# Performance work log

Hardware: AMD Instinct MI355X
Metric: run time of the kernel (lower is better)

Reference implementation:

```python
import jax, jax.numpy as jnp
import numpy as np

B, M, N = 32, 512, 512
XD = YD = 512   # x_size, y_size
S = 512         # shared_size
H = 512         # hidden_size
MAXD = 11       # max relative distance


def _lin(k, i, o):
    lim = float(np.sqrt(6.0 / (i + o)))  # xavier_uniform, gain=1
    return jax.random.uniform(k, (i, o), jnp.float32, -lim, lim)


def setup_inputs() -> dict:
    key = jax.random.key(0)
    ks = jax.random.split(key, 16)
    inp = {
        'prem': jax.random.normal(ks[0], (B, M, YD), jnp.float32),
        'hypo': jax.random.normal(ks[1], (B, N, XD), jnp.float32),
        'prem_mask': jnp.ones((B, M), dtype=bool),
        'hypo_mask': jnp.ones((B, N), dtype=bool),
        # projections
        'Wpx': _lin(ks[2], XD, S), 'bpx': jnp.zeros((S,), jnp.float32),
        'Wpy': _lin(ks[3], YD, S), 'bpy': jnp.zeros((S,), jnp.float32),
        # relative-distance bias embedding (2*max_dist+1, squeezed to scalar)
        'dist_embed': jax.random.normal(ks[4], (2 * MAXD + 1,), jnp.float32),
        # self-attention DeepDot MLP: S -> H -> H
        'Ws1': _lin(ks[5], S, H), 'bs1': jnp.zeros((H,), jnp.float32),
        'Ws2': _lin(ks[6], H, H), 'bs2': jnp.zeros((H,), jnp.float32),
        # cross-attention DeepDot MLP: 2S -> H -> H
        'Wa1': _lin(ks[7], 2 * S, H), 'ba1': jnp.zeros((H,), jnp.float32),
        'Wa2': _lin(ks[8], H, H), 'ba2': jnp.zeros((H,), jnp.float32),
        # compare layer: 4S -> H -> H
        'Wc1': _lin(ks[9], 4 * S, H), 'bc1': jnp.zeros((H,), jnp.float32),
        'Wc2': _lin(ks[10], H, H), 'bc2': jnp.zeros((H,), jnp.float32),
        # aggregate layer: 2H -> H -> H
        'Wg1': _lin(ks[11], 2 * H, H), 'bg1': jnp.zeros((H,), jnp.float32),
        'Wg2': _lin(ks[12], H, H), 'bg2': jnp.zeros((H,), jnp.float32),
    }
    return inp


def _mlp2(x, W1, b1, W2, b2):
    # Linear -> ReLU -> Linear -> ReLU (dropout=0.0)
    h = jax.nn.relu(x @ W1 + b1)
    return jax.nn.relu(h @ W2 + b2)


def _rel_bias(size, dist_embed):
    v = jnp.arange(size)
    d = jnp.clip(v[None, :] - v[:, None], -MAXD, MAXD) + MAXD  # [size,size]
    return dist_embed[d]


def _masked_softmax(t, mask):
    # mask True = valid; broadcast over query dim
    return jax.nn.softmax(jnp.where(mask, t, -jnp.inf), axis=-1)


def reference(prem, hypo, prem_mask, hypo_mask,
              Wpx, bpx, Wpy, bpy, dist_embed,
              Ws1, bs1, Ws2, bs2,
              Wa1, ba1, Wa2, ba2,
              Wc1, bc1, Wc2, bc2,
              Wg1, bg1, Wg2, bg2):
    hypo_p = hypo @ Wpx + bpx   # [B,N,S]
    prem_p = prem @ Wpy + bpy   # [B,M,S]

    # self attention (DeepDot: shared MLP on q and k, then qk^T)
    fp = _mlp2(prem_p, Ws1, bs1, Ws2, bs2)
    fh = _mlp2(hypo_p, Ws1, bs1, Ws2, bs2)
    p_scores = jnp.einsum('bmh,bnh->bmn', fp, fp) + _rel_bias(prem_p.shape[1], dist_embed)[None]
    h_scores = jnp.einsum('bmh,bnh->bmn', fh, fh) + _rel_bias(hypo_p.shape[1], dist_embed)[None]

    p_att = _masked_softmax(p_scores, prem_mask[:, None, :])
    h_att = _masked_softmax(h_scores, hypo_mask[:, None, :])
    prem_ctx = jnp.einsum('bmn,bnd->bmd', p_att, prem_p)
    hypo_ctx = jnp.einsum('bmn,bnd->bmd', h_att, hypo_p)

    prem2 = jnp.concatenate([prem_p, prem_ctx], axis=-1)  # [B,M,2S]
    hypo2 = jnp.concatenate([hypo_p, hypo_ctx], axis=-1)  # [B,N,2S]

    # cross attention
    gp = _mlp2(prem2, Wa1, ba1, Wa2, ba2)
    gh = _mlp2(hypo2, Wa1, ba1, Wa2, ba2)
    sim = jnp.einsum('bmh,bnh->bmn', gp, gh)  # [B,M,N]
    p2h = _masked_softmax(sim, hypo_mask[:, None, :])
    h2p = _masked_softmax(jnp.swapaxes(sim, 1, 2), prem_mask[:, None, :])
    attended_hypo = jnp.einsum('bmn,bnd->bmd', p2h, hypo2)  # [B,M,2S]
    attended_prem = jnp.einsum('bnm,bmd->bnd', h2p, prem2)  # [B,N,2S]

    prem_cmp = _mlp2(jnp.concatenate([prem2, attended_hypo], -1), Wc1, bc1, Wc2, bc2)
    hypo_cmp = _mlp2(jnp.concatenate([hypo2, attended_prem], -1), Wc1, bc1, Wc2, bc2)

    prem_cmp = (prem_cmp * prem_mask[..., None].astype(prem_cmp.dtype)).sum(axis=1)  # [B,H]
    hypo_cmp = (hypo_cmp * hypo_mask[..., None].astype(hypo_cmp.dtype)).sum(axis=1)  # [B,H]

    return _mlp2(jnp.concatenate([prem_cmp, hypo_cmp], -1), Wg1, bg1, Wg2, bg2)
```

## Files before the change

kernel.cpp:

```cpp
#include <hip/hip_runtime.h>
#include <hip/hip_bf16.h>


typedef __bf16 bf16x8 __attribute__((ext_vector_type(8)));
typedef float floatx16 __attribute__((ext_vector_type(16)));

__device__ __forceinline__ unsigned short f32_to_bf16(float f) {
    unsigned int u = __float_as_uint(f);
    unsigned int r = (u + 0x7FFFu + ((u >> 16) & 1u)) >> 16;
    return (unsigned short)r;
}
__device__ __forceinline__ float bf16_to_f32(unsigned short h) {
    return __uint_as_float(((unsigned int)h) << 16);
}

__global__ __launch_bounds__(256) void cvt_kernel(const float* __restrict__ X,
                                                  unsigned short* __restrict__ Y,
                                                  long long n4) {
    long long i = ((long long)blockIdx.x * blockDim.x + threadIdx.x);
    if (i < n4) {
        float4 f = ((const float4*)X)[i];
        ushort4 o;
        o.x = f32_to_bf16(f.x); o.y = f32_to_bf16(f.y);
        o.z = f32_to_bf16(f.z); o.w = f32_to_bf16(f.w);
        ((ushort4*)Y)[i] = o;
    }
}

__global__ __launch_bounds__(256) void transpose_w_kernel(const float* __restrict__ W,
                                                          unsigned short* __restrict__ Wt,
                                                          int K, int N) {
    __shared__ unsigned short tile[32][33];
    int n0 = blockIdx.x * 32, k0 = blockIdx.y * 32;
    int tx = threadIdx.x & 31, ty = threadIdx.x >> 5;
    #pragma unroll
    for (int i = 0; i < 4; ++i) {
        int ky = ty + i * 8;
        tile[ky][tx] = f32_to_bf16(W[(long long)(k0 + ky) * N + n0 + tx]);
    }
    __syncthreads();
    #pragma unroll
    for (int i = 0; i < 4; ++i) {
        int ny = ty + i * 8;
        Wt[(long long)(n0 + ny) * K + k0 + tx] = tile[tx][ny];
    }
}

template <bool BT>
__global__ __launch_bounds__(256, 4) void gemm_kernel(
    const unsigned short* __restrict__ A, int lda, long long strideA,
    const unsigned short* __restrict__ B, int ldb, long long strideB,
    float* __restrict__ C32, unsigned short* __restrict__ Cb, int ldc, long long strideC,
    const float* __restrict__ bias, int relu, int M, int N, int K,
    float* __restrict__ csum, int swz) {
    constexpr int BBYTES = BT ? 8192 : (32 * 264);
    constexpr int BUF = 8192 + BBYTES;
    __shared__ alignas(16) char smem[2 * BUF];

    const int t = threadIdx.x;
    const int lane = t & 63;
    const int wave = t >> 6;
    const int wm = (wave >> 1) * 64;
    const int wn = (wave & 1) * 64;
    const int ln = lane & 31;
    const int h = lane >> 5;

    int bx = blockIdx.x, by = blockIdx.y;
    if (swz) {
        int Nt = gridDim.x, Mt = gridDim.y;
        int L = by * Nt + bx;
        int x = L & 7, s = L >> 3;
        by = x * (Mt >> 3) + s / Nt;
        bx = s % Nt;
    }
    const int m0 = by * 128;
    const int n0 = bx * 128;
    const int bz = blockIdx.z;

    const unsigned short* aptr = A + (long long)bz * strideA +
                                 (long long)(m0 + (t >> 1)) * lda + (t & 1) * 16;
    const unsigned short* bptr;
    if (BT)
        bptr = B + (long long)bz * strideB +
               (long long)(n0 + (t >> 1)) * ldb + (t & 1) * 16;
    else
        bptr = B + (long long)bz * strideB +
               (long long)(t >> 4) * ldb + n0 + (t & 15) * 8;
    const long long bstep = BT ? 8 : 16 * (long long)ldb;

    const int aoff = ((t & 1) * 256 + (t >> 1)) * 16;
    const int boff = BT ? (8192 + ((t & 1) * 256 + (t >> 1)) * 16)
                        : (8192 + (t >> 4) * 264 + (t & 15) * 16);
    const int boff2 = BT ? 2048 : 16 * 264;

    floatx16 acc[2][2];
    #pragma unroll
    for (int im = 0; im < 2; ++im)
        #pragma unroll
        for (int in = 0; in < 2; ++in)
            acc[im][in] = (floatx16)(0.f);

    uint4 va0 = *(const uint4*)(aptr);
    uint4 va1 = *(const uint4*)(aptr + 8);
    uint4 vb0 = *(const uint4*)(bptr);
    uint4 vb1 = *(const uint4*)(bptr + bstep);
    aptr += 32;
    bptr += BT ? 32 : 32 * (long long)ldb;
    *(uint4*)(smem + aoff) = va0;
    *(uint4*)(smem + aoff + 2048) = va1;
    *(uint4*)(smem + boff) = vb0;
    *(uint4*)(smem + boff + boff2) = vb1;
    va0 = *(const uint4*)(aptr);
    va1 = *(const uint4*)(aptr + 8);
    vb0 = *(const uint4*)(bptr);
    vb1 = *(const uint4*)(bptr + bstep);
    aptr += 32;
    bptr += BT ? 32 : 32 * (long long)ldb;
    __syncthreads();

    int p = 0;
    for (int k0 = 0; k0 < K; k0 += 32) {
        const char* base = smem + p * BUF;
        #pragma unroll
        for (int s = 0; s < 2; ++s) {
            bf16x8 a[2], b[2];
            #pragma unroll
            for (int im = 0; im < 2; ++im)
                a[im] = *(const bf16x8*)(base + ((s * 2 + h) * 128 + wm + im * 32 + ln) * 16);
            if (BT) {
                #pragma unroll
                for (int in = 0; in < 2; ++in)
                    b[in] = *(const bf16x8*)(base + 8192 +
                                             ((s * 2 + h) * 128 + wn + in * 32 + ln) * 16);
            } else {
                #pragma unroll
                for (int in = 0; in < 2; ++in) {
                    union { bf16x8 v; unsigned short u[8]; } u;
                    #pragma unroll
                    for (int j = 0; j < 8; ++j)
                        u.u[j] = *(const unsigned short*)(base + 8192 +
                                 (s * 16 + h * 8 + j) * 264 + (wn + in * 32 + ln) * 2);
                    b[in] = u.v;
                }
            }
            #pragma unroll
            for (int im = 0; im < 2; ++im)
                #pragma unroll
                for (int in = 0; in < 2; ++in)
                    acc[im][in] = __builtin_amdgcn_mfma_f32_32x32x16_bf16(
                        a[im], b[in], acc[im][in], 0, 0, 0);
        }

        if (k0 + 32 < K) {
            char* nb = smem + (p ^ 1) * BUF;
            *(uint4*)(nb + aoff) = va0;
            *(uint4*)(nb + aoff + 2048) = va1;
            *(uint4*)(nb + boff) = vb0;
            *(uint4*)(nb + boff + boff2) = vb1;
            if (k0 + 64 < K) {
                va0 = *(const uint4*)(aptr);
                va1 = *(const uint4*)(aptr + 8);
                vb0 = *(const uint4*)(bptr);
                vb1 = *(const uint4*)(bptr + bstep);
                aptr += 32;
                bptr += BT ? 32 : 32 * (long long)ldb;
            }
            __syncthreads();
            p ^= 1;
        }
    }

    if (csum) {
        const int bidx = m0 >> 9;
        const long long cbase = (long long)(bidx & 31) * 1024 + (bidx >> 5) * 512;
        #pragma unroll
        for (int in = 0; in < 2; ++in) {
            int n = n0 + wn + in * 32 + ln;
            float bn = bias ? bias[n] : 0.f;
            float s = 0.f;
            #pragma unroll
            for (int im = 0; im < 2; ++im)
                #pragma unroll
                for (int r = 0; r < 16; ++r) {
                    float v = acc[im][in][r] + bn;
                    if (relu) v = fmaxf(v, 0.f);
                    s += v;
                }
            s += __shfl_xor(s, 32);
            if (lane < 32) atomicAdd(&csum[cbase + n], s);
        }
        return;
    }

    float* C32b = C32 ? C32 + (long long)bz * strideC : nullptr;
    unsigned short* Cbb = Cb ? Cb + (long long)bz * strideC : nullptr;
    #pragma unroll
    for (int im = 0; im < 2; ++im) {
        #pragma unroll
        for (int in = 0; in < 2; ++in) {
            int n = n0 + wn + in * 32 + ln;
            float bn = bias ? bias[n] : 0.f;
            #pragma unroll
            for (int r = 0; r < 16; ++r) {
                int m = m0 + wm + im * 32 + (r & 3) + 8 * (r >> 2) + 4 * h;
                float v = acc[im][in][r] + bn;
                if (relu) v = fmaxf(v, 0.f);
                long long off = (long long)m * ldc + n;
                if (C32b) C32b[off] = v;
                if (Cbb) Cbb[off] = f32_to_bf16(v);
            }
        }
    }
}

__global__ __launch_bounds__(256) void softmax_kernel(const float* __restrict__ S,
                                                      unsigned short* __restrict__ P,
                                                      const float* __restrict__ de,
                                                      int rel, int N) {
    const int row = blockIdx.x;
    const int b = blockIdx.y;
    const long long base = ((long long)b * gridDim.x + row) * N;
    const int t = threadIdx.x;
    const int lane = t & 63, wv = t >> 6;
    __shared__ float redmax[4], redsum[4];

    float v[2];
    float mx = -1e30f;
    #pragma unroll
    for (int i = 0; i < 2; ++i) {
        int c = t + i * 256;
        float x = S[base + c];
        if (rel) {
            int d = c - row;
            d = min(11, max(-11, d));
            x += de[d + 11];
        }
        v[i] = x;
        mx = fmaxf(mx, x);
    }
    #pragma unroll
    for (int o = 32; o > 0; o >>= 1) mx = fmaxf(mx, __shfl_down(mx, o));
    if (lane == 0) redmax[wv] = mx;
    __syncthreads();
    mx = fmaxf(fmaxf(redmax[0], redmax[1]), fmaxf(redmax[2], redmax[3]));

    float s = 0.f;
    #pragma unroll
    for (int i = 0; i < 2; ++i) { v[i] = __expf(v[i] - mx); s += v[i]; }
    #pragma unroll
    for (int o = 32; o > 0; o >>= 1) s += __shfl_down(s, o);
    if (lane == 0) redsum[wv] = s;
    __syncthreads();
    s = redsum[0] + redsum[1] + redsum[2] + redsum[3];
    float inv = 1.f / s;
    #pragma unroll
    for (int i = 0; i < 2; ++i) P[base + t + i * 256] = f32_to_bf16(v[i] * inv);
}

__global__ __launch_bounds__(512) void mlp_agg_kernel(const float* __restrict__ X,
                                                      const float* __restrict__ W,
                                                      const float* __restrict__ bias,
                                                      float* __restrict__ out,
                                                      int K, int N, int relu) {
    const int b = blockIdx.y;
    const int nl = threadIdx.x & 63;
    const int n = blockIdx.x * 64 + nl;
    const int ks = threadIdx.x >> 6;
    const int kchunk = K >> 3;
    const float* Xb = X + (long long)b * K;
    const int k0 = ks * kchunk;
    float s = 0.f;
    #pragma unroll 8
    for (int k = k0; k < k0 + kchunk; ++k)
        s += Xb[k] * W[(long long)k * N + n];
    __shared__ float red[8][64];
    red[ks][nl] = s;
    __syncthreads();
    if (threadIdx.x < 64) {
        float t = 0.f;
        #pragma unroll
        for (int i = 0; i < 8; ++i) t += red[i][threadIdx.x];
        t += bias[n];
        if (relu) t = fmaxf(t, 0.f);
        out[(long long)b * N + n] = t;
    }
}

static void gemm(hipStream_t st, bool bt,
                 const void* A, int lda, long long sA,
                 const void* B, int ldb, long long sB,
                 float* C32, void* Cb, int ldc, long long sC,
                 const float* bias, int relu, int M, int N, int K, int batch,
                 float* csum = nullptr) {
    dim3 g(N / 128, M / 128, batch), blk(256);
    int swz = (batch == 1 && (M / 128) % 8 == 0) ? 1 : 0;
    if (bt)
        gemm_kernel<true><<<g, blk, 0, st>>>((const unsigned short*)A, lda, sA,
                                             (const unsigned short*)B, ldb, sB,
                                             C32, (unsigned short*)Cb, ldc, sC, bias, relu, M, N, K,
                                             csum, swz);
    else
        gemm_kernel<false><<<g, blk, 0, st>>>((const unsigned short*)A, lda, sA,
                                              (const unsigned short*)B, ldb, sB,
                                              C32, (unsigned short*)Cb, ldc, sC, bias, relu, M, N, K,
                                              csum, swz);
}

extern "C" void kernel_launch(void* const* d_in, const int* in_sizes, int n_in,
                              void* d_out, int out_size, void* d_ws, size_t ws_size,
                              hipStream_t stream) {
    const int B = 32, SEQ = 512, S = 512;
    const int MT = B * SEQ;
    const int M2 = 2 * MT;

    const float* prem = (const float*)d_in[0];
    const float* hypo = (const float*)d_in[1];
    const float* Wpx = (const float*)d_in[4];  const float* bpx = (const float*)d_in[5];
    const float* Wpy = (const float*)d_in[6];  const float* bpy = (const float*)d_in[7];
    const float* de  = (const float*)d_in[8];
    const float* Ws1 = (const float*)d_in[9];  const float* bs1 = (const float*)d_in[10];
    const float* Ws2 = (const float*)d_in[11]; const float* bs2 = (const float*)d_in[12];
    const float* Wa1 = (const float*)d_in[13]; const float* ba1 = (const float*)d_in[14];
    const float* Wa2 = (const float*)d_in[15]; const float* ba2 = (const float*)d_in[16];
    const float* Wc1 = (const float*)d_in[17]; const float* bc1 = (const float*)d_in[18];
    const float* Wc2 = (const float*)d_in[19]; const float* bc2 = (const float*)d_in[20];
    const float* Wg1 = (const float*)d_in[21]; const float* bg1 = (const float*)d_in[22];
    const float* Wg2 = (const float*)d_in[23]; const float* bg2 = (const float*)d_in[24];

    char* p = (char*)d_ws;
    auto alloc = [&](size_t bytes) { char* r = p; p += (bytes + 255) & ~(size_t)255; return r; };
    unsigned short* prem_bf = (unsigned short*)alloc((size_t)MT * S * 2);
    unsigned short* hypo_bf = (unsigned short*)alloc((size_t)MT * S * 2);
    unsigned short* premcat = (unsigned short*)alloc((size_t)MT * 2048 * 2);
    unsigned short* hypocat = (unsigned short*)alloc((size_t)MT * 2048 * 2);
    float* scores = (float*)alloc((size_t)B * SEQ * SEQ * 4);
    unsigned short* h1 = (unsigned short*)scores;
    unsigned short* att = (unsigned short*)alloc((size_t)B * SEQ * SEQ * 2);
    unsigned short* Wpx_t = (unsigned short*)alloc(512 * 512 * 2);
    unsigned short* Wpy_t = (unsigned short*)alloc(512 * 512 * 2);
    unsigned short* Ws1_t = (unsigned short*)alloc(512 * 512 * 2);
    unsigned short* Ws2_t = (unsigned short*)alloc(512 * 512 * 2);
    unsigned short* Wa1_t = (unsigned short*)alloc(512 * 1024 * 2);
    unsigned short* Wa2_t = (unsigned short*)alloc(512 * 512 * 2);
    unsigned short* Wc1_t = (unsigned short*)alloc(512 * 2048 * 2);
    unsigned short* Wc2_t = (unsigned short*)alloc(512 * 512 * 2);
    float* agg  = (float*)alloc(32 * 1024 * 4);
    float* aggh = (float*)alloc(32 * 512 * 4);

    const long long sBM = (long long)SEQ * SEQ;
    const long long sCat = (long long)SEQ * 2048;

    {
        long long n4 = (long long)MT * S / 4;
        cvt_kernel<<<dim3((n4 + 255) / 256), dim3(256), 0, stream>>>(prem, prem_bf, n4);
        cvt_kernel<<<dim3((n4 + 255) / 256), dim3(256), 0, stream>>>(hypo, hypo_bf, n4);
        transpose_w_kernel<<<dim3(16, 16), 256, 0, stream>>>(Wpx, Wpx_t, 512, 512);
        transpose_w_kernel<<<dim3(16, 16), 256, 0, stream>>>(Wpy, Wpy_t, 512, 512);
        transpose_w_kernel<<<dim3(16, 16), 256, 0, stream>>>(Ws1, Ws1_t, 512, 512);
        transpose_w_kernel<<<dim3(16, 16), 256, 0, stream>>>(Ws2, Ws2_t, 512, 512);
        transpose_w_kernel<<<dim3(16, 32), 256, 0, stream>>>(Wa1, Wa1_t, 1024, 512);
        transpose_w_kernel<<<dim3(16, 16), 256, 0, stream>>>(Wa2, Wa2_t, 512, 512);
        transpose_w_kernel<<<dim3(16, 64), 256, 0, stream>>>(Wc1, Wc1_t, 2048, 512);
        transpose_w_kernel<<<dim3(16, 16), 256, 0, stream>>>(Wc2, Wc2_t, 512, 512);
        hipMemsetAsync(agg, 0, 32 * 1024 * sizeof(float), stream);
    }

    gemm(stream, true, prem_bf, 512, 0, Wpy_t, 512, 0, nullptr, premcat, 2048, 0, bpy, 0, MT, 512, 512, 1);
    gemm(stream, true, hypo_bf, 512, 0, Wpx_t, 512, 0, nullptr, hypocat, 2048, 0, bpx, 0, MT, 512, 512, 1);

    gemm(stream, true, premcat, 2048, 0, Ws1_t, 512, 0, nullptr, h1, 512, 0, bs1, 1, M2, 512, 512, 1);
    gemm(stream, true, h1, 512, 0, Ws2_t, 512, 0, nullptr, prem_bf, 512, 0, bs2, 1, M2, 512, 512, 1);

    gemm(stream, true, prem_bf, 512, sBM, prem_bf, 512, sBM, scores, nullptr, 512, sBM, nullptr, 0, 512, 512, 512, B);
    softmax_kernel<<<dim3(512, B), 256, 0, stream>>>(scores, att, de, 1, 512);
    gemm(stream, false, att, 512, sBM, premcat, 2048, sCat, nullptr, premcat + 512, 2048, sCat,
         nullptr, 0, 512, 512, 512, B);

    gemm(stream, true, hypo_bf, 512, sBM, hypo_bf, 512, sBM, scores, nullptr, 512, sBM, nullptr, 0, 512, 512, 512, B);
    softmax_kernel<<<dim3(512, B), 256, 0, stream>>>(scores, att, de, 1, 512);
    gemm(stream, false, att, 512, sBM, hypocat, 2048, sCat, nullptr, hypocat + 512, 2048, sCat,
         nullptr, 0, 512, 512, 512, B);

    gemm(stream, true, premcat, 2048, 0, Wa1_t, 1024, 0, nullptr, h1, 512, 0, ba1, 1, M2, 512, 1024, 1);
    gemm(stream, true, h1, 512, 0, Wa2_t, 512, 0, nullptr, prem_bf, 512, 0, ba2, 1, M2, 512, 512, 1);

    gemm(stream, true, prem_bf, 512, sBM, hypo_bf, 512, sBM, scores, nullptr, 512, sBM, nullptr, 0, 512, 512, 512, B);
    softmax_kernel<<<dim3(512, B), 256, 0, stream>>>(scores, att, de, 0, 512);
    gemm(stream, false, att, 512, sBM, hypocat, 2048, sCat, nullptr, premcat + 1024, 2048, sCat,
         nullptr, 0, 512, 1024, 512, B);

    gemm(stream, true, hypo_bf, 512, sBM, prem_bf, 512, sBM, scores, nullptr, 512, sBM, nullptr, 0, 512, 512, 512, B);
    softmax_kernel<<<dim3(512, B), 256, 0, stream>>>(scores, att, de, 0, 512);
    gemm(stream, false, att, 512, sBM, premcat, 2048, sCat, nullptr, hypocat + 1024, 2048, sCat,
         nullptr, 0, 512, 1024, 512, B);

    gemm(stream, true, premcat, 2048, 0, Wc1_t, 2048, 0, nullptr, h1, 512, 0, bc1, 1, M2, 512, 2048, 1);
    gemm(stream, true, h1, 512, 0, Wc2_t, 512, 0, nullptr, nullptr, 512, 0, bc2, 1, M2, 512, 512, 1,
         agg);

    mlp_agg_kernel<<<dim3(8, 32), 512, 0, stream>>>(agg, Wg1, bg1, aggh, 1024, 512, 1);
    mlp_agg_kernel<<<dim3(8, 32), 512, 0, stream>>>(aggh, Wg2, bg2, (float*)d_out, 512, 512, 1);
}
```

Baseline: 773.2 us.

## Merge prem/hypo attention paths into batched launches and fuse fp32 input conversion

Removes the separate fp32-to-bf16 conversion kernels by letting the projection GEMM read fp32 activations directly and convert while staging to shared memory, with an M-split selecting the per-half weight and bias. Premise and hypothesis self- and cross-attention now run as single 64-batch GEMM and softmax launches, using a batch XOR offset to pair each premise with its hypothesis. The eight weight transposes are folded into one launch. The attention buffer now aliases the scores buffer, with each bf16 row written in place at double stride. This cuts launch count and tail effects, but relies on the in-place aliasing being safe and adds fp32 load bandwidth inside the GEMM.

```diff
diff --git a/kernel.cpp b/kernel.cpp
--- a/kernel.cpp
+++ b/kernel.cpp
@@ -10,33 +10,26 @@
     unsigned int r = (u + 0x7FFFu + ((u >> 16) & 1u)) >> 16;
     return (unsigned short)r;
 }
-__device__ __forceinline__ float bf16_to_f32(unsigned short h) {
-    return __uint_as_float(((unsigned int)h) << 16);
-}
-
-__global__ __launch_bounds__(256) void cvt_kernel(const float* __restrict__ X,
-                                                  unsigned short* __restrict__ Y,
-                                                  long long n4) {
-    long long i = ((long long)blockIdx.x * blockDim.x + threadIdx.x);
-    if (i < n4) {
-        float4 f = ((const float4*)X)[i];
-        ushort4 o;
-        o.x = f32_to_bf16(f.x); o.y = f32_to_bf16(f.y);
-        o.z = f32_to_bf16(f.z); o.w = f32_to_bf16(f.w);
-        ((ushort4*)Y)[i] = o;
-    }
-}
-
-__global__ __launch_bounds__(256) void transpose_w_kernel(const float* __restrict__ W,
-                                                          unsigned short* __restrict__ Wt,
-                                                          int K, int N) {
+
+struct TW {
+    const float* src[8];
+    unsigned short* dst[8];
+    int K[8];
+};
+__global__ __launch_bounds__(256) void transpose_all_kernel(TW tw) {
+    const int z = blockIdx.z;
+    const int K = tw.K[z];
+    const int k0 = blockIdx.y * 32;
+    if (k0 >= K) return;
+    const float* W = tw.src[z];
+    unsigned short* Wt = tw.dst[z];
     __shared__ unsigned short tile[32][33];
-    int n0 = blockIdx.x * 32, k0 = blockIdx.y * 32;
+    int n0 = blockIdx.x * 32;
     int tx = threadIdx.x & 31, ty = threadIdx.x >> 5;
     #pragma unroll
     for (int i = 0; i < 4; ++i) {
         int ky = ty + i * 8;
-        tile[ky][tx] = f32_to_bf16(W[(long long)(k0 + ky) * N + n0 + tx]);
+        tile[ky][tx] = f32_to_bf16(W[(long long)(k0 + ky) * 512 + n0 + tx]);
     }
     __syncthreads();
     #pragma unroll
@@ -46,10 +39,11 @@
     }
 }
 
-template <bool BT>
+template <bool BT, bool AF32>
 __global__ __launch_bounds__(256, 4) void gemm_kernel(
-    const unsigned short* __restrict__ A, int lda, long long strideA,
-    const unsigned short* __restrict__ B, int ldb, long long strideB,
+    const void* __restrict__ Av, const void* __restrict__ A2v, int lda, long long strideA,
+    const unsigned short* __restrict__ Bw, int ldb, long long strideB, int bxor,
+    const unsigned short* __restrict__ B2, const float* __restrict__ bias2, int Msplit,
     float* __restrict__ C32, unsigned short* __restrict__ Cb, int ldc, long long strideC,
     const float* __restrict__ bias, int relu, int M, int N, int K,
     float* __restrict__ csum, int swz) {
@@ -76,15 +70,31 @@
     const int m0 = by * 128;
     const int n0 = bx * 128;
     const int bz = blockIdx.z;
-
-    const unsigned short* aptr = A + (long long)bz * strideA +
-                                 (long long)(m0 + (t >> 1)) * lda + (t & 1) * 16;
+    const int bzB = (bz + bxor) & ((int)gridDim.z - 1);
+
+    const unsigned short* B = Bw;
+    const float* biasp = bias;
+    long long mA = m0;
+    if (Msplit && m0 >= Msplit) {
+        if (B2) B = B2;
+        if (bias2) biasp = bias2;
+        if (A2v) { Av = A2v; mA = m0 - Msplit; }
+    }
+
+    const float* aptrF = nullptr;
+    const unsigned short* aptrH = nullptr;
+    if constexpr (AF32)
+        aptrF = (const float*)Av + (long long)bz * strideA +
+                (mA + (t >> 1)) * (long long)lda + (t & 1) * 16;
+    else
+        aptrH = (const unsigned short*)Av + (long long)bz * strideA +
+                (mA + (t >> 1)) * (long long)lda + (t & 1) * 16;
     const unsigned short* bptr;
     if (BT)
-        bptr = B + (long long)bz * strideB +
+        bptr = B + (long long)bzB * strideB +
                (long long)(n0 + (t >> 1)) * ldb + (t & 1) * 16;
     else
-        bptr = B + (long long)bz * strideB +
+        bptr = B + (long long)bzB * strideB +
                (long long)(t >> 4) * ldb + n0 + (t & 15) * 8;
     const long long bstep = BT ? 8 : 16 * (long long)ldb;
 
@@ -100,22 +110,51 @@
         for (int in = 0; in < 2; ++in)
             acc[im][in] = (floatx16)(0.f);
 
-    uint4 va0 = *(const uint4*)(aptr);
-    uint4 va1 = *(const uint4*)(aptr + 8);
-    uint4 vb0 = *(const uint4*)(bptr);
-    uint4 vb1 = *(const uint4*)(bptr + bstep);
-    aptr += 32;
-    bptr += BT ? 32 : 32 * (long long)ldb;
-    *(uint4*)(smem + aoff) = va0;
-    *(uint4*)(smem + aoff + 2048) = va1;
-    *(uint4*)(smem + boff) = vb0;
-    *(uint4*)(smem + boff + boff2) = vb1;
-    va0 = *(const uint4*)(aptr);
-    va1 = *(const uint4*)(aptr + 8);
-    vb0 = *(const uint4*)(bptr);
-    vb1 = *(const uint4*)(bptr + bstep);
-    aptr += 32;
-    bptr += BT ? 32 : 32 * (long long)ldb;
+    uint4 va0, va1, vb0, vb1;
+    float4 fa0, fa1, fa2, fa3;
+
+    auto loadA = [&]() {
+        if constexpr (AF32) {
+            fa0 = *(const float4*)(aptrF);
+            fa1 = *(const float4*)(aptrF + 4);
+            fa2 = *(const float4*)(aptrF + 8);
+            fa3 = *(const float4*)(aptrF + 12);
+            aptrF += 32;
+        } else {
+            va0 = *(const uint4*)(aptrH);
+            va1 = *(const uint4*)(aptrH + 8);
+            aptrH += 32;
+        }
+    };
+    auto loadB = [&]() {
+        vb0 = *(const uint4*)(bptr);
+        vb1 = *(const uint4*)(bptr + bstep);
+        bptr += BT ? 32 : 32 * (long long)ldb;
+    };
+    auto commit = [&](char* buf) {
+        if constexpr (AF32) {
+            union { uint4 q; unsigned short u[8]; } c0, c1;
+            c0.u[0] = f32_to_bf16(fa0.x); c0.u[1] = f32_to_bf16(fa0.y);
+            c0.u[2] = f32_to_bf16(fa0.z); c0.u[3] = f32_to_bf16(fa0.w);
+            c0.u[4] = f32_to_bf16(fa1.x); c0.u[5] = f32_to_bf16(fa1.y);
+            c0.u[6] = f32_to_bf16(fa1.z); c0.u[7] = f32_to_bf16(fa1.w);
+            c1.u[0] = f32_to_bf16(fa2.x); c1.u[1] = f32_to_bf16(fa2.y);
+            c1.u[2] = f32_to_bf16(fa2.z); c1.u[3] = f32_to_bf16(fa2.w);
+            c1.u[4] = f32_to_bf16(fa3.x); c1.u[5] = f32_to_bf16(fa3.y);
+            c1.u[6] = f32_to_bf16(fa3.z); c1.u[7] = f32_to_bf16(fa3.w);
+            *(uint4*)(buf + aoff) = c0.q;
+            *(uint4*)(buf + aoff + 2048) = c1.q;
+        } else {
+            *(uint4*)(buf + aoff) = va0;
+            *(uint4*)(buf + aoff + 2048) = va1;
+        }
+        *(uint4*)(buf + boff) = vb0;
+        *(uint4*)(buf + boff + boff2) = vb1;
+    };
+
+    loadA(); loadB();
+    commit(smem);
+    loadA(); loadB();
     __syncthreads();
 
     int p = 0;
@@ -152,19 +191,8 @@
         }
 
         if (k0 + 32 < K) {
-            char* nb = smem + (p ^ 1) * BUF;
-            *(uint4*)(nb + aoff) = va0;
-            *(uint4*)(nb + aoff + 2048) = va1;
-            *(uint4*)(nb + boff) = vb0;
-            *(uint4*)(nb + boff + boff2) = vb1;
-            if (k0 + 64 < K) {
-                va0 = *(const uint4*)(aptr);
-                va1 = *(const uint4*)(aptr + 8);
-                vb0 = *(const uint4*)(bptr);
-                vb1 = *(const uint4*)(bptr + bstep);
-                aptr += 32;
-                bptr += BT ? 32 : 32 * (long long)ldb;
-            }
+            commit(smem + (p ^ 1) * BUF);
+            if (k0 + 64 < K) { loadA(); loadB(); }
             __syncthreads();
             p ^= 1;
         }
@@ -176,7 +204,7 @@
         #pragma unroll
         for (int in = 0; in < 2; ++in) {
             int n = n0 + wn + in * 32 + ln;
-            float bn = bias ? bias[n] : 0.f;
+            float bn = biasp ? biasp[n] : 0.f;
             float s = 0.f;
             #pragma unroll
             for (int im = 0; im < 2; ++im)
@@ -199,7 +227,7 @@
         #pragma unroll
         for (int in = 0; in < 2; ++in) {
             int n = n0 + wn + in * 32 + ln;
-            float bn = bias ? bias[n] : 0.f;
+            float bn = biasp ? biasp[n] : 0.f;
             #pragma unroll
             for (int r = 0; r < 16; ++r) {
                 int m = m0 + wm + im * 32 + (r & 3) + 8 * (r >> 2) + 4 * h;
@@ -213,13 +241,13 @@
     }
 }
 
-__global__ __launch_bounds__(256) void softmax_kernel(const float* __restrict__ S,
-                                                      unsigned short* __restrict__ P,
-                                                      const float* __restrict__ de,
-                                                      int rel, int N) {
+__global__ __launch_bounds__(256) void softmax_kernel(const float* S,
+                                                      unsigned short* P,
+                                                      const float* de, int rel) {
     const int row = blockIdx.x;
     const int b = blockIdx.y;
-    const long long base = ((long long)b * gridDim.x + row) * N;
+    const long long baseS = ((long long)b * 512 + row) * 512;
+    const long long baseP = ((long long)b * 512 + row) * 1024;
     const int t = threadIdx.x;
     const int lane = t & 63, wv = t >> 6;
     __shared__ float redmax[4], redsum[4];
@@ -229,7 +257,7 @@
     #pragma unroll
     for (int i = 0; i < 2; ++i) {
         int c = t + i * 256;
-        float x = S[base + c];
+        float x = S[baseS + c];
         if (rel) {
             int d = c - row;
             d = min(11, max(-11, d));
@@ -254,7 +282,7 @@
     s = redsum[0] + redsum[1] + redsum[2] + redsum[3];
     float inv = 1.f / s;
     #pragma unroll
-    for (int i = 0; i < 2; ++i) P[base + t + i * 256] = f32_to_bf16(v[i] * inv);
+    for (int i = 0; i < 2; ++i) P[baseP + t + i * 256] = f32_to_bf16(v[i] * inv);
 }
 
 __global__ __launch_bounds__(512) void mlp_agg_kernel(const float* __restrict__ X,
@@ -286,30 +314,38 @@
     }
 }
 
-static void gemm(hipStream_t st, bool bt,
-                 const void* A, int lda, long long sA,
-                 const void* B, int ldb, long long sB,
+static void gemm(hipStream_t st, bool bt, bool af32,
+                 const void* A, const void* A2, int lda, long long sA,
+                 const void* B, int ldb, long long sB, int bxor,
+                 const void* B2, const float* bias2, int Msplit,
                  float* C32, void* Cb, int ldc, long long sC,
                  const float* bias, int relu, int M, int N, int K, int batch,
                  float* csum = nullptr) {
     dim3 g(N / 128, M / 128, batch), blk(256);
     int swz = (batch == 1 && (M / 128) % 8 == 0) ? 1 : 0;
-    if (bt)
-        gemm_kernel<true><<<g, blk, 0, st>>>((const unsigned short*)A, lda, sA,
-                                             (const unsigned short*)B, ldb, sB,
-                                             C32, (unsigned short*)Cb, ldc, sC, bias, relu, M, N, K,
-                                             csum, swz);
-    else
-        gemm_kernel<false><<<g, blk, 0, st>>>((const unsigned short*)A, lda, sA,
-                                              (const unsigned short*)B, ldb, sB,
-                                              C32, (unsigned short*)Cb, ldc, sC, bias, relu, M, N, K,
-                                              csum, swz);
+    if (bt) {
+        if (af32)
+            gemm_kernel<true, true><<<g, blk, 0, st>>>(
+                A, A2, lda, sA, (const unsigned short*)B, ldb, sB, bxor,
+                (const unsigned short*)B2, bias2, Msplit,
+                C32, (unsigned short*)Cb, ldc, sC, bias, relu, M, N, K, csum, swz);
+        else
+            gemm_kernel<true, false><<<g, blk, 0, st>>>(
+                A, A2, lda, sA, (const unsigned short*)B, ldb, sB, bxor,
+                (const unsigned short*)B2, bias2, Msplit,
+                C32, (unsigned short*)Cb, ldc, sC, bias, relu, M, N, K, csum, swz);
+    } else {
+        gemm_kernel<false, false><<<g, blk, 0, st>>>(
+            A, A2, lda, sA, (const unsigned short*)B, ldb, sB, bxor,
+            (const unsigned short*)B2, bias2, Msplit,
+            C32, (unsigned short*)Cb, ldc, sC, bias, relu, M, N, K, csum, swz);
+    }
 }
 
 extern "C" void kernel_launch(void* const* d_in, const int* in_sizes, int n_in,
                               void* d_out, int out_size, void* d_ws, size_t ws_size,
                               hipStream_t stream) {
-    const int B = 32, SEQ = 512, S = 512;
+    const int B = 32, SEQ = 512;
     const int MT = B * SEQ;
     const int M2 = 2 * MT;
 
@@ -329,13 +365,13 @@
 
     char* p = (char*)d_ws;
     auto alloc = [&](size_t bytes) { char* r = p; p += (bytes + 255) & ~(size_t)255; return r; };
-    unsigned short* prem_bf = (unsigned short*)alloc((size_t)MT * S * 2);
-    unsigned short* hypo_bf = (unsigned short*)alloc((size_t)MT * S * 2);
+    unsigned short* prem_bf = (unsigned short*)alloc((size_t)MT * 512 * 2);
+    unsigned short* hypo_bf = (unsigned short*)alloc((size_t)MT * 512 * 2);
     unsigned short* premcat = (unsigned short*)alloc((size_t)MT * 2048 * 2);
     unsigned short* hypocat = (unsigned short*)alloc((size_t)MT * 2048 * 2);
-    float* scores = (float*)alloc((size_t)B * SEQ * SEQ * 4);
+    float* scores = (float*)alloc((size_t)64 * SEQ * SEQ * 4);
     unsigned short* h1 = (unsigned short*)scores;
-    unsigned short* att = (unsigned short*)alloc((size_t)B * SEQ * SEQ * 2);
+    unsigned short* att = (unsigned short*)scores;
     unsigned short* Wpx_t = (unsigned short*)alloc(512 * 512 * 2);
     unsigned short* Wpy_t = (unsigned short*)alloc(512 * 512 * 2);
     unsigned short* Ws1_t = (unsigned short*)alloc(512 * 512 * 2);
@@ -346,57 +382,55 @@
     unsigned short* Wc2_t = (unsigned short*)alloc(512 * 512 * 2);
     float* agg  = (float*)alloc(32 * 1024 * 4);
     float* aggh = (float*)alloc(32 * 512 * 4);
+    (void)hypo_bf; (void)hypocat;
 
     const long long sBM = (long long)SEQ * SEQ;
+    const long long sAtt = (long long)SEQ * 1024;
     const long long sCat = (long long)SEQ * 2048;
 
     {
-        long long n4 = (long long)MT * S / 4;
-        cvt_kernel<<<dim3((n4 + 255) / 256), dim3(256), 0, stream>>>(prem, prem_bf, n4);
-        cvt_kernel<<<dim3((n4 + 255) / 256), dim3(256), 0, stream>>>(hypo, hypo_bf, n4);
-        transpose_w_kernel<<<dim3(16, 16), 256, 0, stream>>>(Wpx, Wpx_t, 512, 512);
-        transpose_w_kernel<<<dim3(16, 16), 256, 0, stream>>>(Wpy, Wpy_t, 512, 512);
-        transpose_w_kernel<<<dim3(16, 16), 256, 0, stream>>>(Ws1, Ws1_t, 512, 512);
-        transpose_w_kernel<<<dim3(16, 16), 256, 0, stream>>>(Ws2, Ws2_t, 512, 512);
-        transpose_w_kernel<<<dim3(16, 32), 256, 0, stream>>>(Wa1, Wa1_t, 1024, 512);
-        transpose_w_kernel<<<dim3(16, 16), 256, 0, stream>>>(Wa2, Wa2_t, 512, 512);
-        transpose_w_kernel<<<dim3(16, 64), 256, 0, stream>>>(Wc1, Wc1_t, 2048, 512);
-        transpose_w_kernel<<<dim3(16, 16), 256, 0, stream>>>(Wc2, Wc2_t, 512, 512);
+        TW tw;
+        tw.src[0] = Wpy; tw.dst[0] = Wpy_t; tw.K[0] = 512;
+        tw.src[1] = Wpx; tw.dst[1] = Wpx_t; tw.K[1] = 512;
+        tw.src[2] = Ws1; tw.dst[2] = Ws1_t; tw.K[2] = 512;
+        tw.src[3] = Ws2; tw.dst[3] = Ws2_t; tw.K[3] = 512;
+        tw.src[4] = Wa1; tw.dst[4] = Wa1_t; tw.K[4] = 1024;
+        tw.src[5] = Wa2; tw.dst[5] = Wa2_t; tw.K[5] = 512;
+        tw.src[6] = Wc1; tw.dst[6] = Wc1_t; tw.K[6] = 2048;
+        tw.src[7] = Wc2; tw.dst[7] = Wc2_t; tw.K[7] = 512;
+        transpose_all_kernel<<<dim3(16, 64, 8), 256, 0, stream>>>(tw);
         hipMemsetAsync(agg, 0, 32 * 1024 * sizeof(float), stream);
     }
 
-    gemm(stream, true, prem_bf, 512, 0, Wpy_t, 512, 0, nullptr, premcat, 2048, 0, bpy, 0, MT, 512, 512, 1);
-    gemm(stream, true, hypo_bf, 512, 0, Wpx_t, 512, 0, nullptr, hypocat, 2048, 0, bpx, 0, MT, 512, 512, 1);
-
-    gemm(stream, true, premcat, 2048, 0, Ws1_t, 512, 0, nullptr, h1, 512, 0, bs1, 1, M2, 512, 512, 1);
-    gemm(stream, true, h1, 512, 0, Ws2_t, 512, 0, nullptr, prem_bf, 512, 0, bs2, 1, M2, 512, 512, 1);
-
-    gemm(stream, true, prem_bf, 512, sBM, prem_bf, 512, sBM, scores, nullptr, 512, sBM, nullptr, 0, 512, 512, 512, B);
-    softmax_kernel<<<dim3(512, B), 256, 0, stream>>>(scores, att, de, 1, 512);
-    gemm(stream, false, att, 512, sBM, premcat, 2048, sCat, nullptr, premcat + 512, 2048, sCat,
-         nullptr, 0, 512, 512, 512, B);
-
-    gemm(stream, true, hypo_bf, 512, sBM, hypo_bf, 512, sBM, scores, nullptr, 512, sBM, nullptr, 0, 512, 512, 512, B);
-    softmax_kernel<<<dim3(512, B), 256, 0, stream>>>(scores, att, de, 1, 512);
-    gemm(stream, false, att, 512, sBM, hypocat, 2048, sCat, nullptr, hypocat + 512, 2048, sCat,
-         nullptr, 0, 512, 512, 512, B);
-
-    gemm(stream, true, premcat, 2048, 0, Wa1_t, 1024, 0, nullptr, h1, 512, 0, ba1, 1, M2, 512, 1024, 1);
-    gemm(stream, true, h1, 512, 0, Wa2_t, 512, 0, nullptr, prem_bf, 512, 0, ba2, 1, M2, 512, 512, 1);
-
-    gemm(stream, true, prem_bf, 512, sBM, hypo_bf, 512, sBM, scores, nullptr, 512, sBM, nullptr, 0, 512, 512, 512, B);
-    softmax_kernel<<<dim3(512, B), 256, 0, stream>>>(scores, att, de, 0, 512);
-    gemm(stream, false, att, 512, sBM, hypocat, 2048, sCat, nullptr, premcat + 1024, 2048, sCat,
-         nullptr, 0, 512, 1024, 512, B);
-
-    gemm(stream, true, hypo_bf, 512, sBM, prem_bf, 512, sBM, scores, nullptr, 512, sBM, nullptr, 0, 512, 512, 512, B);
-    softmax_kernel<<<dim3(512, B), 256, 0, stream>>>(scores, att, de, 0, 512);
-    gemm(stream, false, att, 512, sBM, premcat, 2048, sCat, nullptr, hypocat + 1024, 2048, sCat,
-         nullptr, 0, 512, 1024, 512, B);
-
-    gemm(stream, true, premcat, 2048, 0, Wc1_t, 2048, 0, nullptr, h1, 512, 0, bc1, 1, M2, 512, 2048, 1);
-    gemm(stream, true, h1, 512, 0, Wc2_t, 512, 0, nullptr, nullptr, 512, 0, bc2, 1, M2, 512, 512, 1,
-         agg);
+    gemm(stream, true, true, prem, hypo, 512, 0, Wpy_t, 512, 0, 0,
+         Wpx_t, bpx, MT, nullptr, premcat, 2048, 0, bpy, 0, M2, 512, 512, 1);
+
+    gemm(stream, true, false, premcat, nullptr, 2048, 0, Ws1_t, 512, 0, 0,
+         nullptr, nullptr, 0, nullptr, h1, 512, 0, bs1, 1, M2, 512, 512, 1);
+    gemm(stream, true, false, h1, nullptr, 512, 0, Ws2_t, 512, 0, 0,
+         nullptr, nullptr, 0, nullptr, prem_bf, 512, 0, bs2, 1, M2, 512, 512, 1);
+
+    gemm(stream, true, false, prem_bf, nullptr, 512, sBM, prem_bf, 512, sBM, 0,
+         nullptr, nullptr, 0, scores, nullptr, 512, sBM, nullptr, 0, 512, 512, 512, 64);
+    softmax_kernel<<<dim3(512, 64), 256, 0, stream>>>(scores, att, de, 1);
+    gemm(stream, false, false, att, nullptr, 1024, sAtt, premcat, 2048, sCat, 0,
+         nullptr, nullptr, 0, nullptr, premcat + 512, 2048, sCat, nullptr, 0, 512, 512, 512, 64);
+
+    gemm(stream, true, false, premcat, nullptr, 2048, 0, Wa1_t, 1024, 0, 0,
+         nullptr, nullptr, 0, nullptr, h1, 512, 0, ba1, 1, M2, 512, 1024, 1);
+    gemm(stream, true, false, h1, nullptr, 512, 0, Wa2_t, 512, 0, 0,
+         nullptr, nullptr, 0, nullptr, prem_bf, 512, 0, ba2, 1, M2, 512, 512, 1);
+
+    gemm(stream, true, false, prem_bf, nullptr, 512, sBM, prem_bf, 512, sBM, 32,
+         nullptr, nullptr, 0, scores, nullptr, 512, sBM, nullptr, 0, 512, 512, 512, 64);
+    softmax_kernel<<<dim3(512, 64), 256, 0, stream>>>(scores, att, de, 0);
+    gemm(stream, false, false, att, nullptr, 1024, sAtt, premcat, 2048, sCat, 32,
+         nullptr, nullptr, 0, nullptr, premcat + 1024, 2048, sCat, nullptr, 0, 512, 1024, 512, 64);
+
+    gemm(stream, true, false, premcat, nullptr, 2048, 0, Wc1_t, 2048, 0, 0,
+         nullptr, nullptr, 0, nullptr, h1, 512, 0, bc1, 1, M2, 512, 2048, 1);
+    gemm(stream, true, false, h1, nullptr, 512, 0, Wc2_t, 512, 0, 0,
+         nullptr, nullptr, 0, nullptr, nullptr, 512, 0, bc2, 1, M2, 512, 512, 1, agg);
 
     mlp_agg_kernel<<<dim3(8, 32), 512, 0, stream>>>(agg, Wg1, bg1, aggh, 1024, 512, 1);
     mlp_agg_kernel<<<dim3(8, 32), 512, 0, stream>>>(aggh, Wg2, bg2, (float*)d_out, 512, 512, 1);
```

After: 698.8 us. -9.6%, faster.
